# Kernel tuning notes

Hardware: AMD Instinct MI355X
Metric: run time of the kernel (lower is better)

The kernel has to match this reference:

```python
import jax, jax.numpy as jnp
import numpy as np

SEG = 4      # segment_size
H = 8        # n_heads
D = 1024     # d_model
B = 8
S = 4096


def setup_inputs() -> dict:
    key = jax.random.key(0)
    ks = jax.random.split(key, 9)
    s = 0.02  # init scale for weights
    return {
        "x": jax.random.normal(ks[0], (B, S, D), dtype=jnp.float32),
        "proj_qk_w": jax.random.normal(ks[1], (D, D), dtype=jnp.float32) * s,
        "proj_qk_b": jax.random.normal(ks[2], (D,), dtype=jnp.float32) * s,
        "proj_v_w": jax.random.normal(ks[3], (D, D), dtype=jnp.float32) * s,
        "proj_v_b": jax.random.normal(ks[4], (D,), dtype=jnp.float32) * s,
        "in_proj_w": jax.random.normal(ks[5], (3 * D, D), dtype=jnp.float32) * s,
        "in_proj_b": jax.random.normal(ks[6], (3 * D,), dtype=jnp.float32) * s,
        "out_proj_w": jax.random.normal(ks[7], (D, D), dtype=jnp.float32) * s,
        "out_proj_b": jax.random.normal(ks[8], (D,), dtype=jnp.float32) * s,
    }


def reference(x, proj_qk_w, proj_qk_b, proj_v_w, proj_v_b,
              in_proj_w, in_proj_b, out_proj_w, out_proj_b):
    b, seq_len, d = x.shape
    hd = d // H
    # torch: pad = seg - S % seg  (pads a full segment when S % seg == 0)
    pad = SEG - seq_len % SEG
    x = jnp.concatenate([x, x[:, :pad]], axis=1)          # [b, T, d]
    T = seq_len + pad
    a = T // SEG
    # cat(chunk(x, a, dim=1), dim=0): block-major stacking -> [a*b, SEG, d]
    xb = x.reshape(b, a, SEG, d).transpose(1, 0, 2, 3).reshape(a * b, SEG, d)

    # extra projections (same qk projection used for query and key)
    qk_in = xb @ proj_qk_w.T + proj_qk_b                   # [a*b, SEG, d]
    v_in = xb @ proj_v_w.T + proj_v_b

    # nn.MultiheadAttention in-projection
    wq, wk, wv = jnp.split(in_proj_w, 3, axis=0)
    bq, bk, bv = jnp.split(in_proj_b, 3)
    q = (qk_in @ wq.T + bq).reshape(a * b, SEG, H, hd)
    k = (qk_in @ wk.T + bk).reshape(a * b, SEG, H, hd)
    v = (v_in @ wv.T + bv).reshape(a * b, SEG, H, hd)

    scale = 1.0 / np.sqrt(hd).astype(np.float32)
    scores = jnp.einsum('nqhd,nkhd->nhqk', q * scale, k)   # [a*b, H, SEG, SEG]
    # diagonal exclusion mask (True on the diagonal = masked)
    diag = jnp.eye(SEG, dtype=bool)
    scores = jnp.where(diag[None, None], jnp.finfo(scores.dtype).min, scores)
    attn = jax.nn.softmax(scores, axis=-1)
    o = jnp.einsum('nhqk,nkhd->nqhd', attn, v).reshape(a * b, SEG, d)
    o = o @ out_proj_w.T + out_proj_b                      # [a*b, SEG, d]

    # cat(chunk(x, a, dim=0), dim=1): invert the block stacking
    out = o.reshape(a, b, SEG, d).transpose(1, 0, 2, 3).reshape(b, T, d)
    return out[:, :seq_len]
```

## Files before the change

### kernel.cpp

```cpp
#include <hip/hip_runtime.h>
#include <hip/hip_bf16.h>

typedef __bf16 bf16x8 __attribute__((ext_vector_type(8)));
typedef float f32x4 __attribute__((ext_vector_type(4)));

__device__ __forceinline__ float bf2f(unsigned int u) {
    unsigned int x = u << 16;
    return __builtin_bit_cast(float, x);
}
__device__ __forceinline__ unsigned short f2bf(float f) {
    unsigned int x = __builtin_bit_cast(unsigned int, f);
    x += 0x7fffu + ((x >> 16) & 1u);
    return (unsigned short)(x >> 16);
}

__device__ __forceinline__ void gld_lds16(const unsigned short* g, unsigned short* s) {
    __builtin_amdgcn_global_load_lds((const __attribute__((address_space(1))) void*)g,
                                     (__attribute__((address_space(3))) void*)s, 16, 0, 0);
}

template<bool OUT_F32>
__global__ __launch_bounds__(512) void gemm256(
    const unsigned short* __restrict__ A, int lda,
    const unsigned short* __restrict__ B,
    const float* __restrict__ bias,
    void* __restrict__ C, int N, int K, int nbm)
{
    extern __shared__ char smem[];
    const int tid   = threadIdx.x;
    const int lane  = tid & 63;
    const int wave  = tid >> 6;
    const int wm    = (wave >> 2) * 128;
    const int wn    = (wave & 3) * 64;
    const int lrow  = lane & 15;
    const int lquad = lane >> 4;

    int L = (int)blockIdx.x;
    L = (L & 7) * ((int)gridDim.x >> 3) + (L >> 3);
    const long bn = (long)(L / nbm) * 256;
    const long bm = (long)(L % nbm) * 256;

    const int srow = (lane & 7) + ((lane >> 5) << 3);
    const int scol = ((lane >> 3) & 3) * 8;
    const unsigned short* Asrc0 = A + (bm + wave * 16 + srow) * (long)lda + scol;
    const unsigned short* Asrc1 = A + (bm + (8 + wave) * 16 + srow) * (long)lda + scol;
    const unsigned short* Bsrc0 = B + (bn + wave * 16 + srow) * (long)K + scol;
    const unsigned short* Bsrc1 = B + (bn + (8 + wave) * 16 + srow) * (long)K + scol;

    const int dA0 = wave * 1024 + lane * 16;
    const int dA1 = (8 + wave) * 1024 + lane * 16;
    const int dB0 = 16384 + dA0;
    const int dB1 = 16384 + dA1;

    const int rdoff = (lrow & 7) * 16 + (lrow >> 3) * 512 + lquad * 128;

    f32x4 acc[8][4];
#pragma unroll
    for (int i = 0; i < 8; i++)
#pragma unroll
        for (int j = 0; j < 4; j++)
            acc[i][j] = (f32x4){0.f, 0.f, 0.f, 0.f};

    const int NU = K >> 5;

    auto stageA = [&](int su, int slot) {
        char* sb = smem + (size_t)(slot * 32768);
        gld_lds16(Asrc0 + su * 32, (unsigned short*)(sb + dA0));
        gld_lds16(Asrc1 + su * 32, (unsigned short*)(sb + dA1));
    };
    auto stageB = [&](int su, int slot) {
        char* sb = smem + (size_t)(slot * 32768);
        gld_lds16(Bsrc0 + su * 32, (unsigned short*)(sb + dB0));
        gld_lds16(Bsrc1 + su * 32, (unsigned short*)(sb + dB1));
    };

    stageA(0, 0); stageB(0, 0);
    stageA(1, 1); stageB(1, 1);
    stageA(2, 2); stageB(2, 2);
    asm volatile("s_waitcnt vmcnt(8)\n\ts_barrier" ::: "memory");

    for (int u = 0; u < NU; ++u) {
        char* sl = smem + (size_t)((u & 3) * 32768);
        const int us   = (u + 3 < NU) ? (u + 3) : (NU - 1);
        const int slot = (u + 3) & 3;
        bf16x8 af[8], bq[4];

#pragma unroll
        for (int j = 0; j < 4; j++)
            bq[j] = *(const bf16x8*)(sl + 16384 + ((wn >> 4) + j) * 1024 + rdoff);
#pragma unroll
        for (int i = 0; i < 4; i++)
            af[i] = *(const bf16x8*)(sl + ((wm >> 4) + i) * 1024 + rdoff);
        stageA(us, slot);
#pragma unroll
        for (int i = 4; i < 8; i++)
            af[i] = *(const bf16x8*)(sl + ((wm >> 4) + i) * 1024 + rdoff);
        stageB(us, slot);

        __builtin_amdgcn_s_setprio(1);
#pragma unroll
        for (int i = 0; i < 8; i++)
#pragma unroll
            for (int j = 0; j < 4; j++)
                acc[i][j] = __builtin_amdgcn_mfma_f32_16x16x32_bf16(bq[j], af[i], acc[i][j], 0, 0, 0);
        __builtin_amdgcn_s_setprio(0);

        asm volatile("s_waitcnt vmcnt(8)\n\ts_barrier" ::: "memory");
    }

    asm volatile("s_waitcnt vmcnt(0)" ::: "memory");

#pragma unroll
    for (int i = 0; i < 8; i++) {
        const long row = bm + wm + i * 16 + lrow;
#pragma unroll
        for (int j = 0; j < 4; j++) {
            const int colb = (int)bn + wn + j * 16 + lquad * 4;
            float4 b4 = bias ? ((const float4*)bias)[colb >> 2]
                             : make_float4(0.f, 0.f, 0.f, 0.f);
            const float v0 = acc[i][j][0] + b4.x;
            const float v1 = acc[i][j][1] + b4.y;
            const float v2 = acc[i][j][2] + b4.z;
            const float v3 = acc[i][j][3] + b4.w;
            if (OUT_F32) {
                *(float4*)&((float*)C)[row * (long)N + colb] = make_float4(v0, v1, v2, v3);
            } else {
                unsigned int lo = (unsigned int)f2bf(v0) | ((unsigned int)f2bf(v1) << 16);
                unsigned int hi = (unsigned int)f2bf(v2) | ((unsigned int)f2bf(v3) << 16);
                *(uint2*)&((unsigned short*)C)[row * (long)N + colb] = make_uint2(lo, hi);
            }
        }
    }
}

template<bool OUT_F32>
__global__ __launch_bounds__(256) void gemm_bt(
    const unsigned short* __restrict__ A, int lda,
    const unsigned short* __restrict__ B,
    const unsigned short* __restrict__ B2, long bsplit,
    const float* __restrict__ bias,
    void* __restrict__ C, int N, int K)
{
    __shared__ unsigned short As[128 * 32];
    __shared__ unsigned short Bs[128 * 32];
    const int tid   = threadIdx.x;
    const int lane  = tid & 63;
    const int wave  = tid >> 6;
    const int wm    = (wave >> 1) * 64;
    const int wn    = (wave & 1) * 64;
    const int lrow  = lane & 15;
    const int lquad = lane >> 4;
    const long bm = (long)blockIdx.y * 128;
    const long bn = (long)blockIdx.x * 128;
    const unsigned short* Bp = (bm >= bsplit) ? B2 : B;

    f32x4 acc[4][4];
#pragma unroll
    for (int i = 0; i < 4; i++)
#pragma unroll
        for (int j = 0; j < 4; j++)
            acc[i][j] = (f32x4){0.f, 0.f, 0.f, 0.f};

    const int r0 = tid >> 2;
    const int c0 = (tid & 3) * 8;
    const unsigned short* Ag0 = A + (bm + r0) * (long)lda + c0;
    const unsigned short* Ag1 = A + (bm + r0 + 64) * (long)lda + c0;
    const unsigned short* Bg0 = Bp + (bn + r0) * (long)K + c0;
    const unsigned short* Bg1 = Bp + (bn + r0 + 64) * (long)K + c0;
    unsigned short* As0 = &As[tid * 8];
    unsigned short* As1 = &As[tid * 8 + 2048];
    unsigned short* Bs0 = &Bs[tid * 8];
    unsigned short* Bs1 = &Bs[tid * 8 + 2048];

    for (int k0 = 0; k0 < K; k0 += 32) {
        gld_lds16(Ag0 + k0, As0);
        gld_lds16(Ag1 + k0, As1);
        gld_lds16(Bg0 + k0, Bs0);
        gld_lds16(Bg1 + k0, Bs1);
        __syncthreads();
        bf16x8 af[4], bq[4];
#pragma unroll
        for (int i = 0; i < 4; i++)
            af[i] = *(const bf16x8*)&As[(wm + i * 16 + lrow) * 32 + lquad * 8];
#pragma unroll
        for (int j = 0; j < 4; j++)
            bq[j] = *(const bf16x8*)&Bs[(wn + j * 16 + lrow) * 32 + lquad * 8];
#pragma unroll
        for (int i = 0; i < 4; i++)
#pragma unroll
            for (int j = 0; j < 4; j++)
                acc[i][j] = __builtin_amdgcn_mfma_f32_16x16x32_bf16(bq[j], af[i], acc[i][j], 0, 0, 0);
        __syncthreads();
    }

#pragma unroll
    for (int i = 0; i < 4; i++) {
        const long row = bm + wm + i * 16 + lrow;
#pragma unroll
        for (int j = 0; j < 4; j++) {
            const int colb = (int)bn + wn + j * 16 + lquad * 4;
            float4 b4 = bias ? ((const float4*)bias)[colb >> 2]
                             : make_float4(0.f, 0.f, 0.f, 0.f);
            const float v0 = acc[i][j][0] + b4.x;
            const float v1 = acc[i][j][1] + b4.y;
            const float v2 = acc[i][j][2] + b4.z;
            const float v3 = acc[i][j][3] + b4.w;
            if (OUT_F32) {
                *(float4*)&((float*)C)[row * (long)N + colb] = make_float4(v0, v1, v2, v3);
            } else {
                unsigned int lo = (unsigned int)f2bf(v0) | ((unsigned int)f2bf(v1) << 16);
                unsigned int hi = (unsigned int)f2bf(v2) | ((unsigned int)f2bf(v3) << 16);
                *(uint2*)&((unsigned short*)C)[row * (long)N + colb] = make_uint2(lo, hi);
            }
        }
    }
}

__global__ __launch_bounds__(256) void attn4(
    const unsigned short* __restrict__ QKV,
    unsigned short* __restrict__ O)
{
    const int wave = threadIdx.x >> 6;
    const int lane = threadIdx.x & 63;
    const int half = lane >> 5;
    const int l    = lane & 31;
    const int gh = blockIdx.x * 8 + wave * 2 + half;
    const int g = gh >> 3, h = gh & 7;
    const long row0 = (long)g * 4;
    const int d0 = h * 128 + l * 4;
    const float scale = 0.08838834764831845f;

    float q[4][4], k[4][4], v[4][4];
#pragma unroll
    for (int i = 0; i < 4; i++) {
        const unsigned short* base = QKV + (row0 + i) * 3072 + d0;
        uint2 uq = *(const uint2*)base;
        uint2 uk = *(const uint2*)(base + 1024);
        uint2 uv = *(const uint2*)(base + 2048);
        q[i][0] = bf2f(uq.x & 0xffffu); q[i][1] = bf2f(uq.x >> 16);
        q[i][2] = bf2f(uq.y & 0xffffu); q[i][3] = bf2f(uq.y >> 16);
        k[i][0] = bf2f(uk.x & 0xffffu); k[i][1] = bf2f(uk.x >> 16);
        k[i][2] = bf2f(uk.y & 0xffffu); k[i][3] = bf2f(uk.y >> 16);
        v[i][0] = bf2f(uv.x & 0xffffu); v[i][1] = bf2f(uv.x >> 16);
        v[i][2] = bf2f(uv.y & 0xffffu); v[i][3] = bf2f(uv.y >> 16);
    }
    float s[4][4];
#pragma unroll
    for (int i = 0; i < 4; i++)
#pragma unroll
        for (int j = 0; j < 4; j++)
            s[i][j] = q[i][0] * k[j][0] + q[i][1] * k[j][1]
                    + q[i][2] * k[j][2] + q[i][3] * k[j][3];
#pragma unroll
    for (int m = 1; m < 32; m <<= 1)
#pragma unroll
        for (int i = 0; i < 4; i++)
#pragma unroll
            for (int j = 0; j < 4; j++)
                s[i][j] += __shfl_xor(s[i][j], m, 64);

#pragma unroll
    for (int i = 0; i < 4; i++) {
        float mx = -3.0e38f;
#pragma unroll
        for (int j = 0; j < 4; j++)
            if (j != i) mx = fmaxf(mx, s[i][j] * scale);
        float p[4], den = 0.f;
#pragma unroll
        for (int j = 0; j < 4; j++) {
            p[j] = (j == i) ? 0.f : __expf(s[i][j] * scale - mx);
            den += p[j];
        }
        const float inv = 1.f / den;
        float o0 = 0.f, o1 = 0.f, o2 = 0.f, o3 = 0.f;
#pragma unroll
        for (int j = 0; j < 4; j++) {
            const float a = p[j] * inv;
            o0 += a * v[j][0]; o1 += a * v[j][1];
            o2 += a * v[j][2]; o3 += a * v[j][3];
        }
        unsigned int lo = (unsigned int)f2bf(o0) | ((unsigned int)f2bf(o1) << 16);
        unsigned int hi = (unsigned int)f2bf(o2) | ((unsigned int)f2bf(o3) << 16);
        *(uint2*)(O + (row0 + i) * 1024 + d0) = make_uint2(lo, hi);
    }
}

__global__ __launch_bounds__(256) void cvt_bf16(const float* __restrict__ in,
                                                unsigned short* __restrict__ out, int n4)
{
    int i = blockIdx.x * blockDim.x + threadIdx.x;
    if (i >= n4) return;
    float4 v = ((const float4*)in)[i];
    unsigned int a = (unsigned int)f2bf(v.x) | ((unsigned int)f2bf(v.y) << 16);
    unsigned int b = (unsigned int)f2bf(v.z) | ((unsigned int)f2bf(v.w) << 16);
    ((uint2*)out)[i] = make_uint2(a, b);
}

__global__ __launch_bounds__(256) void cvt_weights(const float* __restrict__ win,
                                                   unsigned short* __restrict__ win16,
                                                   const float* __restrict__ wout,
                                                   unsigned short* __restrict__ wo16)
{
    int i = blockIdx.x * blockDim.x + threadIdx.x;
    const float* in;
    unsigned short* out;
    int j;
    if (i < 786432) { in = win; out = win16; j = i; }
    else            { in = wout; out = wo16; j = i - 786432; }
    float4 v = ((const float4*)in)[j];
    unsigned int a = (unsigned int)f2bf(v.x) | ((unsigned int)f2bf(v.y) << 16);
    unsigned int b = (unsigned int)f2bf(v.z) | ((unsigned int)f2bf(v.w) << 16);
    ((uint2*)out)[j] = make_uint2(a, b);
}

__global__ __launch_bounds__(256) void transpose_cvt2(const float* __restrict__ a,
                                                      unsigned short* __restrict__ oa,
                                                      const float* __restrict__ b,
                                                      unsigned short* __restrict__ ob, int n)
{
    const float* in = blockIdx.z ? b : a;
    unsigned short* out = blockIdx.z ? ob : oa;
    __shared__ unsigned short tile[64][65];
    const int bx = blockIdx.x * 64, by = blockIdx.y * 64;
    const int tx = threadIdx.x & 63, ty = threadIdx.x >> 6;
    for (int r = ty; r < 64; r += 4)
        tile[r][tx] = f2bf(in[(long)(by + r) * n + bx + tx]);
    __syncthreads();
    for (int r = ty; r < 64; r += 4)
        out[(long)(bx + r) * n + by + tx] = tile[tx][r];
}

__global__ __launch_bounds__(256) void bias_prep(const float* __restrict__ win,
                                                 const float* __restrict__ bqk,
                                                 const float* __restrict__ bv,
                                                 const float* __restrict__ bin,
                                                 float* __restrict__ bbig)
{
    const int row = blockIdx.x * 4 + (threadIdx.x >> 6);
    const int lane = threadIdx.x & 63;
    const float* b = (row < 2048) ? bqk : bv;
    float s = 0.f;
    for (int t = lane; t < 1024; t += 64) s += win[(long)row * 1024 + t] * b[t];
#pragma unroll
    for (int m = 1; m < 64; m <<= 1) s += __shfl_xor(s, m, 64);
    if (lane == 0) bbig[row] = s + bin[row];
}

extern "C" void kernel_launch(void* const* d_in, const int* in_sizes, int n_in,
                              void* d_out, int out_size, void* d_ws, size_t ws_size,
                              hipStream_t stream)
{
    (void)in_sizes; (void)n_in; (void)out_size; (void)ws_size;
    const float* x    = (const float*)d_in[0];
    const float* wqk  = (const float*)d_in[1];
    const float* bqk  = (const float*)d_in[2];
    const float* wv   = (const float*)d_in[3];
    const float* bv   = (const float*)d_in[4];
    const float* win  = (const float*)d_in[5];
    const float* bin  = (const float*)d_in[6];
    const float* wout = (const float*)d_in[7];
    const float* bout = (const float*)d_in[8];

    char* ws = (char*)d_ws;
    unsigned short* buf0  = (unsigned short*)ws;
    unsigned short* qkv   = (unsigned short*)(ws + (64ll << 20));
    unsigned short* win16 = (unsigned short*)(ws + (256ll << 20));
    unsigned short* wqkT  = (unsigned short*)(ws + (262ll << 20));
    unsigned short* wvT   = (unsigned short*)(ws + (264ll << 20));
    unsigned short* wbig  = (unsigned short*)(ws + (266ll << 20));
    unsigned short* wo16  = (unsigned short*)(ws + (272ll << 20));
    float*          bbig  = (float*)(ws + (274ll << 20));
    unsigned short* o16   = buf0;

    hipFuncSetAttribute(reinterpret_cast<const void*>(&gemm256<false>),
                        hipFuncAttributeMaxDynamicSharedMemorySize, 131072);
    hipFuncSetAttribute(reinterpret_cast<const void*>(&gemm256<true>),
                        hipFuncAttributeMaxDynamicSharedMemorySize, 131072);

    dim3 blk(256);
    cvt_bf16<<<32768, 256, 0, stream>>>(x, buf0, 8388608);
    cvt_weights<<<4096, 256, 0, stream>>>(win, win16, wout, wo16);
    transpose_cvt2<<<dim3(16, 16, 2), blk, 0, stream>>>(wqk, wqkT, wv, wvT, 1024);
    bias_prep<<<768, blk, 0, stream>>>(win, bqk, bv, bin, bbig);

    gemm_bt<false><<<dim3(8, 24), blk, 0, stream>>>(win16, 1024, wqkT, wvT, 2048,
                                                    nullptr, wbig, 1024, 1024);

    gemm256<false><<<dim3(12 * 128), 512, 131072, stream>>>(buf0, 1024, wbig,
                                                            bbig, qkv, 3072, 1024, 128);

    attn4<<<8192, blk, 0, stream>>>(qkv, o16);

    gemm256<true><<<dim3(4 * 128), 512, 131072, stream>>>(o16, 1024, wo16,
                                                          bout, d_out, 1024, 1024, 128);
}
```

Baseline: 698.1 us.

## Replace 256x256 GEMM tiles with 128x128 tiles and 3-stage static LDS pipeline

Switches the main projection GEMMs from 512-thread 256x256 tiles with a 4-deep 128KB dynamic LDS ring to 256-thread 128x128 tiles with a 3-deep 48KB static LDS ring and launch bounds allowing 3 blocks per CU. Block ordering now goes row-major over N tiles instead of M tiles. The goal is higher occupancy and better latency hiding. The cost is lower per-block data reuse, so each output needs more global and LDS traffic.

```diff
diff --git a/kernel.cpp b/kernel.cpp
--- a/kernel.cpp
+++ b/kernel.cpp
@@ -20,98 +20,93 @@
 }
 
 template<bool OUT_F32>
-__global__ __launch_bounds__(512) void gemm256(
+__global__ __launch_bounds__(256, 3) void gemm128(
     const unsigned short* __restrict__ A, int lda,
     const unsigned short* __restrict__ B,
     const float* __restrict__ bias,
-    void* __restrict__ C, int N, int K, int nbm)
-{
-    extern __shared__ char smem[];
+    void* __restrict__ C, int N, int K, int nbn)
+{
+    __shared__ uint4 smem4[3072];
+    char* smem = (char*)smem4;
     const int tid   = threadIdx.x;
     const int lane  = tid & 63;
     const int wave  = tid >> 6;
-    const int wm    = (wave >> 2) * 128;
-    const int wn    = (wave & 3) * 64;
+    const int wm    = (wave >> 1) * 64;
+    const int wn    = (wave & 1) * 64;
     const int lrow  = lane & 15;
     const int lquad = lane >> 4;
 
     int L = (int)blockIdx.x;
     L = (L & 7) * ((int)gridDim.x >> 3) + (L >> 3);
-    const long bn = (long)(L / nbm) * 256;
-    const long bm = (long)(L % nbm) * 256;
+    const long bm = (long)(L / nbn) * 128;
+    const long bn = (long)(L % nbn) * 128;
 
     const int srow = (lane & 7) + ((lane >> 5) << 3);
     const int scol = ((lane >> 3) & 3) * 8;
-    const unsigned short* Asrc0 = A + (bm + wave * 16 + srow) * (long)lda + scol;
-    const unsigned short* Asrc1 = A + (bm + (8 + wave) * 16 + srow) * (long)lda + scol;
-    const unsigned short* Bsrc0 = B + (bn + wave * 16 + srow) * (long)K + scol;
-    const unsigned short* Bsrc1 = B + (bn + (8 + wave) * 16 + srow) * (long)K + scol;
+    const unsigned short* Ag0 = A + (bm + wave * 16 + srow) * (long)lda + scol;
+    const unsigned short* Ag1 = A + (bm + (wave + 4) * 16 + srow) * (long)lda + scol;
+    const unsigned short* Bg0 = B + (bn + wave * 16 + srow) * (long)K + scol;
+    const unsigned short* Bg1 = B + (bn + (wave + 4) * 16 + srow) * (long)K + scol;
 
     const int dA0 = wave * 1024 + lane * 16;
-    const int dA1 = (8 + wave) * 1024 + lane * 16;
-    const int dB0 = 16384 + dA0;
-    const int dB1 = 16384 + dA1;
+    const int dA1 = dA0 + 4096;
+    const int dB0 = 8192 + dA0;
+    const int dB1 = 8192 + dA1;
 
     const int rdoff = (lrow & 7) * 16 + (lrow >> 3) * 512 + lquad * 128;
 
-    f32x4 acc[8][4];
-#pragma unroll
-    for (int i = 0; i < 8; i++)
+    f32x4 acc[4][4];
+#pragma unroll
+    for (int i = 0; i < 4; i++)
 #pragma unroll
         for (int j = 0; j < 4; j++)
             acc[i][j] = (f32x4){0.f, 0.f, 0.f, 0.f};
 
     const int NU = K >> 5;
 
-    auto stageA = [&](int su, int slot) {
-        char* sb = smem + (size_t)(slot * 32768);
-        gld_lds16(Asrc0 + su * 32, (unsigned short*)(sb + dA0));
-        gld_lds16(Asrc1 + su * 32, (unsigned short*)(sb + dA1));
+    auto stage = [&](int su, char* sb) {
+        gld_lds16(Ag0 + su * 32, (unsigned short*)(sb + dA0));
+        gld_lds16(Ag1 + su * 32, (unsigned short*)(sb + dA1));
+        gld_lds16(Bg0 + su * 32, (unsigned short*)(sb + dB0));
+        gld_lds16(Bg1 + su * 32, (unsigned short*)(sb + dB1));
     };
-    auto stageB = [&](int su, int slot) {
-        char* sb = smem + (size_t)(slot * 32768);
-        gld_lds16(Bsrc0 + su * 32, (unsigned short*)(sb + dB0));
-        gld_lds16(Bsrc1 + su * 32, (unsigned short*)(sb + dB1));
-    };
-
-    stageA(0, 0); stageB(0, 0);
-    stageA(1, 1); stageB(1, 1);
-    stageA(2, 2); stageB(2, 2);
-    asm volatile("s_waitcnt vmcnt(8)\n\ts_barrier" ::: "memory");
-
+
+    stage(0, smem);
+    stage(1, smem + 16384);
+    asm volatile("s_waitcnt vmcnt(4)\n\ts_barrier" ::: "memory");
+
+    int cs = 0, ws = 2;
     for (int u = 0; u < NU; ++u) {
-        char* sl = smem + (size_t)((u & 3) * 32768);
-        const int us   = (u + 3 < NU) ? (u + 3) : (NU - 1);
-        const int slot = (u + 3) & 3;
-        bf16x8 af[8], bq[4];
-
-#pragma unroll
-        for (int j = 0; j < 4; j++)
-            bq[j] = *(const bf16x8*)(sl + 16384 + ((wn >> 4) + j) * 1024 + rdoff);
+        const char* sl = smem + cs * 16384;
+        char* sw = smem + ws * 16384;
+        const int us = (u + 2 < NU) ? (u + 2) : (NU - 1);
+        bf16x8 af[4], bq[4];
+
+#pragma unroll
+        for (int j = 0; j < 4; j++)
+            bq[j] = *(const bf16x8*)(sl + 8192 + ((wn >> 4) + j) * 1024 + rdoff);
 #pragma unroll
         for (int i = 0; i < 4; i++)
             af[i] = *(const bf16x8*)(sl + ((wm >> 4) + i) * 1024 + rdoff);
-        stageA(us, slot);
-#pragma unroll
-        for (int i = 4; i < 8; i++)
-            af[i] = *(const bf16x8*)(sl + ((wm >> 4) + i) * 1024 + rdoff);
-        stageB(us, slot);
+        stage(us, sw);
 
         __builtin_amdgcn_s_setprio(1);
 #pragma unroll
-        for (int i = 0; i < 8; i++)
+        for (int i = 0; i < 4; i++)
 #pragma unroll
             for (int j = 0; j < 4; j++)
                 acc[i][j] = __builtin_amdgcn_mfma_f32_16x16x32_bf16(bq[j], af[i], acc[i][j], 0, 0, 0);
         __builtin_amdgcn_s_setprio(0);
 
-        asm volatile("s_waitcnt vmcnt(8)\n\ts_barrier" ::: "memory");
+        asm volatile("s_waitcnt vmcnt(4)\n\ts_barrier" ::: "memory");
+        cs = (cs == 2) ? 0 : cs + 1;
+        ws = (ws == 2) ? 0 : ws + 1;
     }
 
     asm volatile("s_waitcnt vmcnt(0)" ::: "memory");
 
 #pragma unroll
-    for (int i = 0; i < 8; i++) {
+    for (int i = 0; i < 4; i++) {
         const long row = bm + wm + i * 16 + lrow;
 #pragma unroll
         for (int j = 0; j < 4; j++) {
@@ -371,11 +366,8 @@
     unsigned short* wo16  = (unsigned short*)(ws + (272ll << 20));
     float*          bbig  = (float*)(ws + (274ll << 20));
     unsigned short* o16   = buf0;
-
-    hipFuncSetAttribute(reinterpret_cast<const void*>(&gemm256<false>),
-                        hipFuncAttributeMaxDynamicSharedMemorySize, 131072);
-    hipFuncSetAttribute(reinterpret_cast<const void*>(&gemm256<true>),
-                        hipFuncAttributeMaxDynamicSharedMemorySize, 131072);
+    const long NOSPLIT = 1ll << 40;
+    (void)NOSPLIT;
 
     dim3 blk(256);
     cvt_bf16<<<32768, 256, 0, stream>>>(x, buf0, 8388608);
@@ -386,11 +378,11 @@
     gemm_bt<false><<<dim3(8, 24), blk, 0, stream>>>(win16, 1024, wqkT, wvT, 2048,
                                                     nullptr, wbig, 1024, 1024);
 
-    gemm256<false><<<dim3(12 * 128), 512, 131072, stream>>>(buf0, 1024, wbig,
-                                                            bbig, qkv, 3072, 1024, 128);
+    gemm128<false><<<dim3(6144), blk, 0, stream>>>(buf0, 1024, wbig,
+                                                   bbig, qkv, 3072, 1024, 24);
 
     attn4<<<8192, blk, 0, stream>>>(qkv, o16);
 
-    gemm256<true><<<dim3(4 * 128), 512, 131072, stream>>>(o16, 1024, wo16,
-                                                          bout, d_out, 1024, 1024, 128);
-}
+    gemm128<true><<<dim3(2048), blk, 0, stream>>>(o16, 1024, wo16,
+                                                  bout, d_out, 1024, 1024, 8);
+}
```

Measured after the change: 861.5 us. 1.23x slower.
